# Kernel tuning notes

Hardware: AMD Instinct MI355X
Metric: run time of the kernel (lower is better)

Reference implementation:

```python
import jax, jax.numpy as jnp
import numpy as np


def setup_inputs() -> dict:
    key = jax.random.key(0)
    k1, k2, k3, k4 = jax.random.split(key, 4)
    B, N, M, D = 32, 512, 512, 1024
    return {
        "x1": jax.random.normal(k1, (B, N, D), dtype=jnp.float32),
        "x2": jax.random.normal(k2, (B, M, D), dtype=jnp.float32),
        "mask1": jax.random.randint(k3, (B, N), 0, 2, dtype=jnp.int32),
        "mask2": jax.random.randint(k4, (B, M), 0, 2, dtype=jnp.int32),
    }


def _masked_attention(x, align, mask):
    # align: [B, Q, K], mask: [B, K] (broadcast over Q, matching tf.tile over seq_len)
    neg_inf = jnp.asarray(-jnp.inf, dtype=align.dtype)
    align = jnp.where(mask[:, None, :] == 0, neg_inf, align)
    attn = jax.nn.softmax(align, axis=-1)  # [B, Q, K]
    return jnp.matmul(attn, x)  # [B, Q, D]


def reference(x1, x2, mask1, mask2):
    # align12[b, n, m] = x1[b, n, :] . x2[b, m, :]
    align12 = jnp.einsum("bnd,bmd->bnm", x1, x2)
    align21 = jnp.transpose(align12, (0, 2, 1))
    x1_coef = _masked_attention(x2, align12, mask2)  # [B, N, D]
    x2_coef = _masked_attention(x1, align21, mask1)  # [B, M, D]
    return (x1_coef, x2_coef)
```

## Files before the change

kernel.cpp:

```cpp
#include <hip/hip_runtime.h>
#include <hip/hip_bf16.h>

#define BB 32
#define NN 512
#define MM 512
#define DD 1024

typedef __attribute__((ext_vector_type(8))) short short8;
typedef __attribute__((ext_vector_type(4))) float f32x4;

#define ASYNC_COPY16(g, l) \
    __builtin_amdgcn_global_load_lds((__attribute__((address_space(1))) void*)(g), \
                                     (__attribute__((address_space(3))) void*)(l), 16, 0, 0)

__device__ inline unsigned short f2bf(float f) {
    unsigned int u = __float_as_uint(f);
    u += 0x7fffu + ((u >> 16) & 1u);
    return (unsigned short)(u >> 16);
}

#define SPLIT1(vv, hh, ll) { unsigned short h_ = f2bf(vv); \
    float hf_ = __uint_as_float((unsigned int)h_ << 16); \
    hh = h_; ll = f2bf((vv) - hf_); }

__global__ __launch_bounds__(256) void convert_split(
    const float* __restrict__ x1, const float* __restrict__ x2,
    unsigned short* __restrict__ x1h, unsigned short* __restrict__ x1l,
    unsigned short* __restrict__ x2h, unsigned short* __restrict__ x2l) {
    size_t g = (size_t)blockIdx.x * 256 + threadIdx.x;
#pragma unroll
    for (int r = 0; r < 2; ++r) {
        size_t idx = g + (size_t)r * 2097152;
        float4 v = ((const float4*)x1)[idx];
        ushort4 hh, ll;
        SPLIT1(v.x, hh.x, ll.x) SPLIT1(v.y, hh.y, ll.y)
        SPLIT1(v.z, hh.z, ll.z) SPLIT1(v.w, hh.w, ll.w)
        ((ushort4*)x1h)[idx] = hh;
        ((ushort4*)x1l)[idx] = ll;
        float4 u = ((const float4*)x2)[idx];
        ushort4 hh2, ll2;
        SPLIT1(u.x, hh2.x, ll2.x) SPLIT1(u.y, hh2.y, ll2.y)
        SPLIT1(u.z, hh2.z, ll2.z) SPLIT1(u.w, hh2.w, ll2.w)
        ((ushort4*)x2h)[idx] = hh2;
        ((ushort4*)x2l)[idx] = ll2;
    }
}

__global__ __launch_bounds__(512, 4) void gemm_align(
    const unsigned short* __restrict__ x1h, const unsigned short* __restrict__ x1l,
    const unsigned short* __restrict__ x2h, const unsigned short* __restrict__ x2l,
    const int* __restrict__ mask1, const int* __restrict__ mask2,
    float* __restrict__ alg,
    float* __restrict__ rp_max, float* __restrict__ rp_sum,
    float* __restrict__ cp_max, float* __restrict__ cp_sum) {
    __shared__ unsigned short S[2][16384];
    int bid = blockIdx.x;
    int nb = (bid & 7) * 64 + (bid >> 3);
    int b = nb >> 4; int tl = nb & 15;
    int nt = tl >> 2, mt = tl & 3;
    int n0 = nt * 128, m0 = mt * 128;
    int t = threadIdx.x; int w = t >> 6; int l = t & 63;
    int lane16 = l & 15, q = l >> 4, q8 = q * 8;
    int wr = (w >> 2) * 64;
    int wc = (w & 3) * 32;
    f32x4 acc[4][2];
#pragma unroll
    for (int i = 0; i < 4; ++i)
#pragma unroll
        for (int j = 0; j < 2; ++j) acc[i][j] = (f32x4){0.f, 0.f, 0.f, 0.f};
    const unsigned short* gs[4];
    int ls[4];
#pragma unroll
    for (int s = 0; s < 4; ++s) {
        int qq = w * 4 + s;
        int row0 = (qq & 7) * 16;
        const unsigned short* base; int lb;
        if (qq < 8)       { base = x1h + ((size_t)b * 512 + n0) * 1024; lb = 0; }
        else if (qq < 16) { base = x1l + ((size_t)b * 512 + n0) * 1024; lb = 4096; }
        else if (qq < 24) { base = x2h + ((size_t)b * 512 + m0) * 1024; lb = 8192; }
        else              { base = x2l + ((size_t)b * 512 + m0) * 1024; lb = 12288; }
        gs[s] = base + (size_t)(row0 + (l >> 2)) * 1024 + (l & 3) * 8;
        ls[s] = lb + row0 * 32 + l * 8;
    }
#pragma unroll
    for (int s = 0; s < 4; ++s)
        ASYNC_COPY16(gs[s], &S[0][ls[s]]);
    __syncthreads();
    int cur = 0;
    for (int kk = 0; kk < 1024; kk += 32) {
        if (kk + 32 < 1024) {
#pragma unroll
            for (int s = 0; s < 4; ++s)
                ASYNC_COPY16(gs[s] + kk + 32, &S[cur ^ 1][ls[s]]);
        }
        const unsigned short* Sb = S[cur];
        short8 ah[4], al[4], bh[2], bl[2];
#pragma unroll
        for (int i = 0; i < 4; ++i) {
            int off = (wr + i * 16 + lane16) * 32 + q8;
            ah[i] = *(const short8*)&Sb[off];
            al[i] = *(const short8*)&Sb[4096 + off];
        }
#pragma unroll
        for (int j = 0; j < 2; ++j) {
            int off = (wc + j * 16 + lane16) * 32 + q8;
            bh[j] = *(const short8*)&Sb[8192 + off];
            bl[j] = *(const short8*)&Sb[12288 + off];
        }
#pragma unroll
        for (int i = 0; i < 4; ++i)
#pragma unroll
            for (int j = 0; j < 2; ++j) {
                acc[i][j] = __builtin_amdgcn_mfma_f32_16x16x32_bf16(ah[i], bh[j], acc[i][j], 0, 0, 0);
                acc[i][j] = __builtin_amdgcn_mfma_f32_16x16x32_bf16(ah[i], bl[j], acc[i][j], 0, 0, 0);
                acc[i][j] = __builtin_amdgcn_mfma_f32_16x16x32_bf16(al[i], bh[j], acc[i][j], 0, 0, 0);
            }
        __syncthreads();
        cur ^= 1;
    }
    float* ob = alg + ((size_t)b * 512 + n0 + wr) * 512 + m0 + wc;
    int q4 = q * 4;
#pragma unroll
    for (int i = 0; i < 4; ++i)
#pragma unroll
        for (int j = 0; j < 2; ++j)
#pragma unroll
            for (int r = 0; r < 4; ++r)
                ob[(size_t)(i * 16 + q4 + r) * 512 + j * 16 + lane16] = acc[i][j][r];
    int mk2[2];
#pragma unroll
    for (int j = 0; j < 2; ++j) mk2[j] = mask2[b * 512 + m0 + wc + j * 16 + lane16];
    int mk1r[4][4];
#pragma unroll
    for (int i = 0; i < 4; ++i)
#pragma unroll
        for (int r = 0; r < 4; ++r) mk1r[i][r] = mask1[b * 512 + n0 + wr + i * 16 + q4 + r];
#pragma unroll
    for (int j = 0; j < 2; ++j) {
        float cm = -3.0e38f;
#pragma unroll
        for (int i = 0; i < 4; ++i)
#pragma unroll
            for (int r = 0; r < 4; ++r)
                if (mk1r[i][r]) cm = fmaxf(cm, acc[i][j][r]);
        cm = fmaxf(cm, __shfl_xor(cm, 16));
        cm = fmaxf(cm, __shfl_xor(cm, 32));
        float cs = 0.f;
#pragma unroll
        for (int i = 0; i < 4; ++i)
#pragma unroll
            for (int r = 0; r < 4; ++r)
                cs += mk1r[i][r] ? __expf(acc[i][j][r] - cm) : 0.f;
        cs += __shfl_xor(cs, 16);
        cs += __shfl_xor(cs, 32);
        if (q == 0) {
            size_t o = ((size_t)b * 8 + nt * 2 + (w >> 2)) * 512 + m0 + wc + j * 16 + lane16;
            cp_max[o] = cm;
            cp_sum[o] = cs;
        }
    }
    float* rmS = (float*)&S[0][0];
    float* rsS = rmS + 512;
#pragma unroll
    for (int i = 0; i < 4; ++i)
#pragma unroll
        for (int r = 0; r < 4; ++r) {
            float v0 = acc[i][0][r], v1 = acc[i][1][r];
            float rm = fmaxf(mk2[0] ? v0 : -3.0e38f, mk2[1] ? v1 : -3.0e38f);
            rm = fmaxf(rm, __shfl_xor(rm, 1));
            rm = fmaxf(rm, __shfl_xor(rm, 2));
            rm = fmaxf(rm, __shfl_xor(rm, 4));
            rm = fmaxf(rm, __shfl_xor(rm, 8));
            float rs = (mk2[0] ? __expf(v0 - rm) : 0.f) + (mk2[1] ? __expf(v1 - rm) : 0.f);
            rs += __shfl_xor(rs, 1);
            rs += __shfl_xor(rs, 2);
            rs += __shfl_xor(rs, 4);
            rs += __shfl_xor(rs, 8);
            if (lane16 == 0) {
                int row = i * 16 + q4 + r;
                rmS[w * 64 + row] = rm;
                rsS[w * 64 + row] = rs;
            }
        }
    __syncthreads();
    if (t < 128) {
        int grp = t >> 6, rloc = t & 63;
        float M = -3.0e38f;
#pragma unroll
        for (int ww = 0; ww < 4; ++ww) M = fmaxf(M, rmS[(grp * 4 + ww) * 64 + rloc]);
        float Ssum = 0.f;
#pragma unroll
        for (int ww = 0; ww < 4; ++ww)
            Ssum += rsS[(grp * 4 + ww) * 64 + rloc] * __expf(rmS[(grp * 4 + ww) * 64 + rloc] - M);
        size_t o = ((size_t)b * 4 + mt) * 512 + n0 + t;
        rp_max[o] = M;
        rp_sum[o] = Ssum;
    }
}

__global__ __launch_bounds__(256) void combine_stats(
    const float* __restrict__ rp_max, const float* __restrict__ rp_sum,
    const float* __restrict__ cp_max, const float* __restrict__ cp_sum,
    float* __restrict__ rowmax, float* __restrict__ rowinv,
    float* __restrict__ colmax, float* __restrict__ colinv) {
    int idx = blockIdx.x * 256 + threadIdx.x;
    if (idx < 16384) {
        int b = idx >> 9, n = idx & 511;
        float M = -3.0e38f;
#pragma unroll
        for (int tt = 0; tt < 4; ++tt) M = fmaxf(M, rp_max[((size_t)b * 4 + tt) * 512 + n]);
        float S = 0.f;
#pragma unroll
        for (int tt = 0; tt < 4; ++tt) {
            size_t o = ((size_t)b * 4 + tt) * 512 + n;
            S += rp_sum[o] * __expf(rp_max[o] - M);
        }
        rowmax[idx] = M;
        rowinv[idx] = 1.0f / S;
    } else {
        int id2 = idx - 16384;
        int b = id2 >> 9, m = id2 & 511;
        float M = -3.0e38f;
#pragma unroll
        for (int tt = 0; tt < 8; ++tt) M = fmaxf(M, cp_max[((size_t)b * 8 + tt) * 512 + m]);
        float S = 0.f;
#pragma unroll
        for (int tt = 0; tt < 8; ++tt) {
            size_t o = ((size_t)b * 8 + tt) * 512 + m;
            S += cp_sum[o] * __expf(cp_max[o] - M);
        }
        colmax[id2] = M;
        colinv[id2] = 1.0f / S;
    }
}

__global__ __launch_bounds__(256) void apply_softmax(
    const float* __restrict__ alg, const int* __restrict__ mask1,
    const int* __restrict__ mask2,
    const float* __restrict__ rowmax, const float* __restrict__ rowinv,
    const float* __restrict__ colmax, const float* __restrict__ colinv,
    unsigned short* __restrict__ attn12, unsigned short* __restrict__ attn21) {
    int bid = blockIdx.x; int b = bid >> 6; int rem = bid & 63;
    int m0 = (rem >> 3) * 64, n0 = (rem & 7) * 64;
    int t = threadIdx.x;
    __shared__ float lds[64 * 65];
    int jj = t & 63; int ii = t >> 6;
    int mk2 = mask2[b * 512 + m0 + jj];
    unsigned short e12[16];
#pragma unroll
    for (int p = 0; p < 16; ++p) {
        int n = ii + p * 4;
        float v = alg[((size_t)b * 512 + n0 + n) * 512 + m0 + jj];
        lds[n * 65 + jj] = v;
        float rm = rowmax[b * 512 + n0 + n];
        float ri = rowinv[b * 512 + n0 + n];
        e12[p] = mk2 ? f2bf(__expf(v - rm) * ri) : (unsigned short)0;
    }
    __syncthreads();
#pragma unroll
    for (int p = 0; p < 16; ++p) {
        int n = ii + p * 4;
        attn12[((size_t)b * 512 + n0 + n) * 512 + m0 + jj] = e12[p];
    }
    int mk1 = mask1[b * 512 + n0 + jj];
#pragma unroll
    for (int p = 0; p < 16; ++p) {
        int mm = ii + p * 4;
        float cm = colmax[b * 512 + m0 + mm];
        float ci = colinv[b * 512 + m0 + mm];
        float v = lds[jj * 65 + mm];
        unsigned short pv = mk1 ? f2bf(__expf(v - cm) * ci) : (unsigned short)0;
        attn21[((size_t)b * 512 + m0 + mm) * 512 + n0 + jj] = pv;
    }
}

__global__ __launch_bounds__(256) void gemm_pv(
    const unsigned short* __restrict__ P, const unsigned short* __restrict__ V,
    float* __restrict__ out) {
    __shared__ unsigned short SA[2][4096];
    __shared__ unsigned int   SB[2][32 * 65];
    int bid = blockIdx.x;
    int nb = (bid & 7) * 128 + (bid >> 3);
    int b = nb >> 5; int rem = nb & 31;
    int n0 = (rem >> 3) * 128, d0 = (rem & 7) * 128;
    int t = threadIdx.x; int w = t >> 6; int l = t & 63;
    int lane16 = l & 15, q = l >> 4, q8 = q * 8;
    int wr = (w >> 1) * 64, wc = (w & 1) * 64;
    f32x4 acc[4][4];
#pragma unroll
    for (int i = 0; i < 4; ++i)
#pragma unroll
        for (int j = 0; j < 4; ++j) acc[i][j] = (f32x4){0.f, 0.f, 0.f, 0.f};
    const unsigned short* gA = P + ((size_t)b * 512 + n0) * 512;
    const unsigned short* gsA[2];
    int ldsa[2];
#pragma unroll
    for (int s = 0; s < 2; ++s) {
        int a = w * 2 + s;
        gsA[s] = gA + (size_t)(a * 16 + (l >> 2)) * 512 + (l & 3) * 8;
        ldsa[s] = a * 512 + l * 8;
    }
    int dch = l & 15;
    int mloc[2]; mloc[0] = w * 4 + q; mloc[1] = mloc[0] + 16;
    const unsigned short* gB0[2];
#pragma unroll
    for (int s = 0; s < 2; ++s)
        gB0[s] = V + (size_t)b * 524288 + (size_t)mloc[s] * 1024 + d0 + dch * 8;
    union U8 { short8 s; unsigned int u[4]; };
    U8 bv[2];
#pragma unroll
    for (int s = 0; s < 2; ++s) bv[s].s = *(const short8*)gB0[s];
#pragma unroll
    for (int s = 0; s < 2; ++s)
        ASYNC_COPY16(gsA[s], &SA[0][ldsa[s]]);
#pragma unroll
    for (int s = 0; s < 2; ++s)
#pragma unroll
        for (int c = 0; c < 4; ++c)
            SB[0][mloc[s] * 65 + dch * 4 + c] = bv[s].u[c];
    __syncthreads();
    int cur = 0;
    for (int kk = 0; kk < 512; kk += 32) {
        int more = (kk + 32 < 512);
        if (more) {
#pragma unroll
            for (int s = 0; s < 2; ++s) bv[s].s = *(const short8*)(gB0[s] + (size_t)(kk + 32) * 1024);
#pragma unroll
            for (int s = 0; s < 2; ++s)
                ASYNC_COPY16(gsA[s] + kk + 32, &SA[cur ^ 1][ldsa[s]]);
        }
        short8 af[4];
#pragma unroll
        for (int i = 0; i < 4; ++i)
            af[i] = *(const short8*)&SA[cur][(wr + i * 16 + lane16) * 32 + q8];
        const unsigned short* Bs = (const unsigned short*)SB[cur];
        short8 bf[4];
#pragma unroll
        for (int j = 0; j < 4; ++j) {
            int col = wc + j * 16 + lane16;
#pragma unroll
            for (int e = 0; e < 8; ++e)
                bf[j][e] = (short)Bs[(q8 + e) * 130 + col];
        }
#pragma unroll
        for (int i = 0; i < 4; ++i)
#pragma unroll
            for (int j = 0; j < 4; ++j)
                acc[i][j] = __builtin_amdgcn_mfma_f32_16x16x32_bf16(af[i], bf[j], acc[i][j], 0, 0, 0);
        if (more) {
#pragma unroll
            for (int s = 0; s < 2; ++s)
#pragma unroll
                for (int c = 0; c < 4; ++c)
                    SB[cur ^ 1][mloc[s] * 65 + dch * 4 + c] = bv[s].u[c];
        }
        __syncthreads();
        cur ^= 1;
    }
    int q4 = q * 4;
#pragma unroll
    for (int i = 0; i < 4; ++i)
#pragma unroll
        for (int j = 0; j < 4; ++j)
#pragma unroll
            for (int r = 0; r < 4; ++r) {
                int rr = n0 + wr + i * 16 + q4 + r;
                int dd = d0 + wc + j * 16 + lane16;
                out[((size_t)b * 512 + rr) * DD + dd] = acc[i][j][r];
            }
}

extern "C" void kernel_launch(void* const* d_in, const int* in_sizes, int n_in,
                              void* d_out, int out_size, void* d_ws, size_t ws_size,
                              hipStream_t stream) {
    const float* x1 = (const float*)d_in[0];
    const float* x2 = (const float*)d_in[1];
    const int* mask1 = (const int*)d_in[2];
    const int* mask2 = (const int*)d_in[3];
    char* ws = (char*)d_ws;
    unsigned short* x1h  = (unsigned short*)(ws);
    unsigned short* x2h  = (unsigned short*)(ws + 33554432UL);
    unsigned short* x1l  = (unsigned short*)(ws + 134217728UL);
    unsigned short* x2l  = (unsigned short*)(ws + 167772160UL);
    float* alg           = (float*)(ws + 201326592UL);
    unsigned short* attn12 = (unsigned short*)(ws + 134217728UL);
    float* rowmax        = (float*)(ws + 150994944UL);
    float* rowinv        = (float*)(ws + 151060480UL);
    float* colmax        = (float*)(ws + 151126016UL);
    float* colinv        = (float*)(ws + 151191552UL);
    unsigned short* attn21 = (unsigned short*)(ws + 167772160UL);
    float* out1 = (float*)d_out;
    float* out2 = out1 + (size_t)BB * NN * DD;
    float* rp_max = (float*)d_out;
    float* rp_sum = rp_max + 65536;
    float* cp_max = rp_sum + 65536;
    float* cp_sum = cp_max + 131072;

    convert_split<<<8192, 256, 0, stream>>>(x1, x2, x1h, x1l, x2h, x2l);
    gemm_align<<<512, 512, 0, stream>>>(x1h, x1l, x2h, x2l, mask1, mask2, alg,
                                        rp_max, rp_sum, cp_max, cp_sum);
    combine_stats<<<128, 256, 0, stream>>>(rp_max, rp_sum, cp_max, cp_sum,
                                           rowmax, rowinv, colmax, colinv);
    apply_softmax<<<2048, 256, 0, stream>>>(alg, mask1, mask2, rowmax, rowinv,
                                            colmax, colinv, attn12, attn21);
    gemm_pv<<<1024, 256, 0, stream>>>(attn12, x2h, out1);
    gemm_pv<<<1024, 256, 0, stream>>>(attn21, x1h, out2);
}
```

Baseline: 408.7 us.

## Use explicit waitcnt barriers, fuse stats combine into softmax, merge PV launches

Replaces __syncthreads in both GEMM main loops with explicit vmcnt waits plus s_barrier, so next-tile async copies can stay in flight across the barrier. Folds the combine_stats kernel into apply_softmax: each block recomputes its 64 row and 64 column stats into shared memory. Merges the two PV GEMM launches into one grid of 2048 blocks. Together these aim to cut launch overhead and memory-wait stalls, at the cost of redundant stat recomputation and fragile hand-written waitcnt counts.

```diff
diff --git a/kernel.cpp b/kernel.cpp
--- a/kernel.cpp
+++ b/kernel.cpp
@@ -85,14 +85,19 @@
 #pragma unroll
     for (int s = 0; s < 4; ++s)
         ASYNC_COPY16(gs[s], &S[0][ls[s]]);
-    __syncthreads();
     int cur = 0;
     for (int kk = 0; kk < 1024; kk += 32) {
         if (kk + 32 < 1024) {
 #pragma unroll
             for (int s = 0; s < 4; ++s)
                 ASYNC_COPY16(gs[s] + kk + 32, &S[cur ^ 1][ls[s]]);
-        }
+            __builtin_amdgcn_sched_barrier(0);
+            asm volatile("s_waitcnt vmcnt(4)" ::: "memory");
+        } else {
+            asm volatile("s_waitcnt vmcnt(0)" ::: "memory");
+        }
+        __builtin_amdgcn_s_barrier();
+        __builtin_amdgcn_sched_barrier(0);
         const unsigned short* Sb = S[cur];
         short8 ah[4], al[4], bh[2], bl[2];
 #pragma unroll
@@ -115,7 +120,8 @@
                 acc[i][j] = __builtin_amdgcn_mfma_f32_16x16x32_bf16(ah[i], bl[j], acc[i][j], 0, 0, 0);
                 acc[i][j] = __builtin_amdgcn_mfma_f32_16x16x32_bf16(al[i], bh[j], acc[i][j], 0, 0, 0);
             }
-        __syncthreads();
+        __builtin_amdgcn_sched_barrier(0);
+        __builtin_amdgcn_s_barrier();
         cur ^= 1;
     }
     float* ob = alg + ((size_t)b * 512 + n0 + wr) * 512 + m0 + wc;
@@ -198,52 +204,43 @@
     }
 }
 
-__global__ __launch_bounds__(256) void combine_stats(
-    const float* __restrict__ rp_max, const float* __restrict__ rp_sum,
-    const float* __restrict__ cp_max, const float* __restrict__ cp_sum,
-    float* __restrict__ rowmax, float* __restrict__ rowinv,
-    float* __restrict__ colmax, float* __restrict__ colinv) {
-    int idx = blockIdx.x * 256 + threadIdx.x;
-    if (idx < 16384) {
-        int b = idx >> 9, n = idx & 511;
-        float M = -3.0e38f;
-#pragma unroll
-        for (int tt = 0; tt < 4; ++tt) M = fmaxf(M, rp_max[((size_t)b * 4 + tt) * 512 + n]);
-        float S = 0.f;
-#pragma unroll
-        for (int tt = 0; tt < 4; ++tt) {
-            size_t o = ((size_t)b * 4 + tt) * 512 + n;
-            S += rp_sum[o] * __expf(rp_max[o] - M);
-        }
-        rowmax[idx] = M;
-        rowinv[idx] = 1.0f / S;
-    } else {
-        int id2 = idx - 16384;
-        int b = id2 >> 9, m = id2 & 511;
-        float M = -3.0e38f;
-#pragma unroll
-        for (int tt = 0; tt < 8; ++tt) M = fmaxf(M, cp_max[((size_t)b * 8 + tt) * 512 + m]);
-        float S = 0.f;
-#pragma unroll
-        for (int tt = 0; tt < 8; ++tt) {
-            size_t o = ((size_t)b * 8 + tt) * 512 + m;
-            S += cp_sum[o] * __expf(cp_max[o] - M);
-        }
-        colmax[id2] = M;
-        colinv[id2] = 1.0f / S;
-    }
-}
-
 __global__ __launch_bounds__(256) void apply_softmax(
     const float* __restrict__ alg, const int* __restrict__ mask1,
     const int* __restrict__ mask2,
-    const float* __restrict__ rowmax, const float* __restrict__ rowinv,
-    const float* __restrict__ colmax, const float* __restrict__ colinv,
+    const float* __restrict__ rp_max, const float* __restrict__ rp_sum,
+    const float* __restrict__ cp_max, const float* __restrict__ cp_sum,
     unsigned short* __restrict__ attn12, unsigned short* __restrict__ attn21) {
     int bid = blockIdx.x; int b = bid >> 6; int rem = bid & 63;
     int m0 = (rem >> 3) * 64, n0 = (rem & 7) * 64;
     int t = threadIdx.x;
     __shared__ float lds[64 * 65];
+    __shared__ float st[4][64];
+    if (t < 64) {
+        int n = n0 + t;
+        float M = -3.0e38f;
+#pragma unroll
+        for (int tt = 0; tt < 4; ++tt) M = fmaxf(M, rp_max[((size_t)b * 4 + tt) * 512 + n]);
+        float Ssum = 0.f;
+#pragma unroll
+        for (int tt = 0; tt < 4; ++tt) {
+            size_t o = ((size_t)b * 4 + tt) * 512 + n;
+            Ssum += rp_sum[o] * __expf(rp_max[o] - M);
+        }
+        st[0][t] = M; st[1][t] = 1.0f / Ssum;
+    } else if (t < 128) {
+        int m = m0 + (t - 64);
+        float M = -3.0e38f;
+#pragma unroll
+        for (int tt = 0; tt < 8; ++tt) M = fmaxf(M, cp_max[((size_t)b * 8 + tt) * 512 + m]);
+        float Ssum = 0.f;
+#pragma unroll
+        for (int tt = 0; tt < 8; ++tt) {
+            size_t o = ((size_t)b * 8 + tt) * 512 + m;
+            Ssum += cp_sum[o] * __expf(cp_max[o] - M);
+        }
+        st[2][t - 64] = M; st[3][t - 64] = 1.0f / Ssum;
+    }
+    __syncthreads();
     int jj = t & 63; int ii = t >> 6;
     int mk2 = mask2[b * 512 + m0 + jj];
     unsigned short e12[16];
@@ -252,9 +249,7 @@
         int n = ii + p * 4;
         float v = alg[((size_t)b * 512 + n0 + n) * 512 + m0 + jj];
         lds[n * 65 + jj] = v;
-        float rm = rowmax[b * 512 + n0 + n];
-        float ri = rowinv[b * 512 + n0 + n];
-        e12[p] = mk2 ? f2bf(__expf(v - rm) * ri) : (unsigned short)0;
+        e12[p] = mk2 ? f2bf(__expf(v - st[0][n]) * st[1][n]) : (unsigned short)0;
     }
     __syncthreads();
 #pragma unroll
@@ -266,20 +261,23 @@
 #pragma unroll
     for (int p = 0; p < 16; ++p) {
         int mm = ii + p * 4;
-        float cm = colmax[b * 512 + m0 + mm];
-        float ci = colinv[b * 512 + m0 + mm];
         float v = lds[jj * 65 + mm];
-        unsigned short pv = mk1 ? f2bf(__expf(v - cm) * ci) : (unsigned short)0;
+        unsigned short pv = mk1 ? f2bf(__expf(v - st[2][mm]) * st[3][mm]) : (unsigned short)0;
         attn21[((size_t)b * 512 + m0 + mm) * 512 + n0 + jj] = pv;
     }
 }
 
-__global__ __launch_bounds__(256) void gemm_pv(
-    const unsigned short* __restrict__ P, const unsigned short* __restrict__ V,
-    float* __restrict__ out) {
+__global__ __launch_bounds__(256) void gemm_pv2(
+    const unsigned short* __restrict__ attn12, const unsigned short* __restrict__ x2h,
+    const unsigned short* __restrict__ attn21, const unsigned short* __restrict__ x1h,
+    float* __restrict__ out1, float* __restrict__ out2) {
     __shared__ unsigned short SA[2][4096];
     __shared__ unsigned int   SB[2][32 * 65];
-    int bid = blockIdx.x;
+    int bid0 = blockIdx.x;
+    const unsigned short* P; const unsigned short* V; float* out;
+    if (bid0 < 1024) { P = attn12; V = x2h; out = out1; }
+    else             { P = attn21; V = x1h; out = out2; }
+    int bid = bid0 & 1023;
     int nb = (bid & 7) * 128 + (bid >> 3);
     int b = nb >> 5; int rem = nb & 31;
     int n0 = (rem >> 3) * 128, d0 = (rem & 7) * 128;
@@ -325,10 +323,17 @@
         if (more) {
 #pragma unroll
             for (int s = 0; s < 2; ++s) bv[s].s = *(const short8*)(gB0[s] + (size_t)(kk + 32) * 1024);
+            __builtin_amdgcn_sched_barrier(0);
 #pragma unroll
             for (int s = 0; s < 2; ++s)
                 ASYNC_COPY16(gsA[s] + kk + 32, &SA[cur ^ 1][ldsa[s]]);
-        }
+            __builtin_amdgcn_sched_barrier(0);
+            asm volatile("s_waitcnt vmcnt(4)" ::: "memory");
+        } else {
+            asm volatile("s_waitcnt vmcnt(0)" ::: "memory");
+        }
+        __builtin_amdgcn_s_barrier();
+        __builtin_amdgcn_sched_barrier(0);
         short8 af[4];
 #pragma unroll
         for (int i = 0; i < 4; ++i)
@@ -354,7 +359,9 @@
                 for (int c = 0; c < 4; ++c)
                     SB[cur ^ 1][mloc[s] * 65 + dch * 4 + c] = bv[s].u[c];
         }
-        __syncthreads();
+        asm volatile("s_waitcnt lgkmcnt(0)" ::: "memory");
+        __builtin_amdgcn_sched_barrier(0);
+        __builtin_amdgcn_s_barrier();
         cur ^= 1;
     }
     int q4 = q * 4;
@@ -384,10 +391,6 @@
     unsigned short* x2l  = (unsigned short*)(ws + 167772160UL);
     float* alg           = (float*)(ws + 201326592UL);
     unsigned short* attn12 = (unsigned short*)(ws + 134217728UL);
-    float* rowmax        = (float*)(ws + 150994944UL);
-    float* rowinv        = (float*)(ws + 151060480UL);
-    float* colmax        = (float*)(ws + 151126016UL);
-    float* colinv        = (float*)(ws + 151191552UL);
     unsigned short* attn21 = (unsigned short*)(ws + 167772160UL);
     float* out1 = (float*)d_out;
     float* out2 = out1 + (size_t)BB * NN * DD;
@@ -399,10 +402,8 @@
     convert_split<<<8192, 256, 0, stream>>>(x1, x2, x1h, x1l, x2h, x2l);
     gemm_align<<<512, 512, 0, stream>>>(x1h, x1l, x2h, x2l, mask1, mask2, alg,
                                         rp_max, rp_sum, cp_max, cp_sum);
-    combine_stats<<<128, 256, 0, stream>>>(rp_max, rp_sum, cp_max, cp_sum,
-                                           rowmax, rowinv, colmax, colinv);
-    apply_softmax<<<2048, 256, 0, stream>>>(alg, mask1, mask2, rowmax, rowinv,
-                                            colmax, colinv, attn12, attn21);
-    gemm_pv<<<1024, 256, 0, stream>>>(attn12, x2h, out1);
-    gemm_pv<<<1024, 256, 0, stream>>>(attn21, x1h, out2);
-}
+    apply_softmax<<<2048, 256, 0, stream>>>(alg, mask1, mask2,
+                                            rp_max, rp_sum, cp_max, cp_sum,
+                                            attn12, attn21);
+    gemm_pv2<<<2048, 256, 0, stream>>>(attn12, x2h, attn21, x1h, out1, out2);
+}
```

After: 381.2 us. -6.7%, faster.
